# Performance work log

Hardware: AMD Instinct MI355X
Metric: run time of the kernel (lower is better)

## Reference

```python
import jax, jax.numpy as jnp
import numpy as np

H, W = 512, 512
K = 10
N_ACTIONS = 8
HID1, HID2, HIDP = 32, 64, 32
# 8-neighborhood directions (i_dot, j_dot), as in env.DIRS
DIRS = [(-1, -1), (-1, 0), (-1, 1), (0, -1), (0, 1), (1, -1), (1, 0), (1, 1)]


def setup_inputs() -> dict:
    key = jax.random.key(0)
    ks = jax.random.split(key, 16)
    n_state = H * W
    w = lambda k, shape: (jax.random.normal(k, shape, dtype=jnp.float32) * 0.02)
    return {
        "x": jax.random.uniform(ks[0], (3, H, W), dtype=jnp.float32),
        "pos": jax.random.randint(ks[1], (2,), 0, H, dtype=jnp.int32),
        "W1": w(ks[2], (HID1, 3 * n_state)), "b1": jnp.zeros((HID1,), jnp.float32),
        "W2": w(ks[3], (HID2, HID1)), "b2": jnp.zeros((HID2,), jnp.float32),
        "Wro": w(ks[4], (n_state, HID2)), "bro": jnp.zeros((n_state,), jnp.float32),
        "Wri": w(ks[5], (n_state, HID2)), "bri": jnp.zeros((n_state,), jnp.float32),
        "Wp": w(ks[6], (n_state, HID2)), "bp": jnp.zeros((n_state,), jnp.float32),
        "Wpol": w(ks[7], (HIDP, 4 * n_state)), "bpol": jnp.zeros((HIDP,), jnp.float32),
        "Whead": w(ks[8], (N_ACTIONS, HIDP)), "bhead": jnp.zeros((N_ACTIONS,), jnp.float32),
    }


def reference(x, pos, W1, b1, W2, b2, Wro, bro, Wri, bri, Wp, bp, Wpol, bpol, Whead, bhead):
    state = x.reshape(-1)  # (3*H*W,)
    h = jax.nn.relu(W1 @ state + b1)
    h = jax.nn.relu(W2 @ h + b2)
    r_out = jax.nn.sigmoid(Wro @ h + bro).reshape(H, W)
    r_in = jax.nn.sigmoid(Wri @ h + bri).reshape(H, W)
    p = jax.nn.sigmoid(Wp @ h + bp).reshape(H, W)

    p_pad = jnp.pad(p, 1)
    rin_pad = jnp.pad(r_in, 1)
    rout_pad = jnp.pad(r_out, 1)

    def step(v, _):
        v_pad = jnp.pad(v, 1)  # (H+2, W+2)
        cands = []
        for i_dot, j_dot in DIRS:
            xs = j_dot + 1  # note: original code uses j_dot along axis 0
            ys = i_dot + 1
            cands.append(
                v_pad[xs:xs + H, ys:ys + W] * p_pad[xs:xs + H, ys:ys + W]
                + rin_pad[xs:xs + H, ys:ys + W] - rout_pad[xs:xs + H, ys:ys + W]
            )
        return jnp.max(jnp.stack(cands, 0), axis=0), None

    v, _ = jax.lax.scan(step, jnp.zeros((H, W), jnp.float32), None, length=K)

    inp_pol = jnp.concatenate([v.reshape(-1), state])  # (4*H*W,)
    logits = Whead @ jax.nn.relu(Wpol @ inp_pol + bpol) + bhead
    action_prob = jax.nn.softmax(logits, axis=-1)
    state_value = v[pos[0], pos[1]]
    return action_prob, state_value
```

## Files before the change

### kernel.cpp

```cpp
#include <hip/hip_runtime.h>

#define HW 512
#define NSTATE (HW * HW)
#define NC4_X 196608
#define NC4_POLROW 262144
#define NC4_V 65536

#define SEG4 1024
#define NSEG_MV 192
#define NSEG_PV 64
#define SPAN_ROP 1024

#define WS_PART1 0
#define WS_PARTPX 6144
#define WS_PARTPV 12288
#define WS_H2 14336
#define WS_P 14400
#define WS_RD (WS_P + NSTATE)
#define WS_V (WS_RD + NSTATE)

#define SGB __builtin_amdgcn_sched_group_barrier

__global__ __launch_bounds__(256) void mv_dual(
    const float4* __restrict__ W1, const float4* __restrict__ Wpol,
    const float4* __restrict__ x, float* __restrict__ part1,
    float* __restrict__ partPx) {
  __shared__ float4 xs[SEG4];
  int b = blockIdx.x;
  int m = b >= 1536;
  if (m) b -= 1536;
  int q = b / NSEG_MV, s = b - q * NSEG_MV;
  int tid = threadIdx.x, wave = tid >> 6, lane = tid & 63;
  const float4* __restrict__ xseg = x + (size_t)s * SEG4;
#pragma unroll
  for (int k = 0; k < 4; ++k) xs[tid + k * 256] = xseg[tid + k * 256];
  __syncthreads();
  int row = q * 4 + wave;
  const float4* __restrict__ wrow =
      (m ? Wpol + NC4_V + (size_t)row * NC4_POLROW
         : W1 + (size_t)row * NC4_X) +
      (size_t)s * SEG4 + lane;
  float acc = 0.f;
#pragma unroll
  for (int bt = 0; bt < 2; ++bt) {
    float4 w[8];
#pragma unroll
    for (int j = 0; j < 8; ++j) w[j] = wrow[bt * 512 + j * 64];
    SGB(0x020, 8, 0);
    float4 xv[8];
#pragma unroll
    for (int j = 0; j < 8; ++j) xv[j] = xs[bt * 512 + j * 64 + lane];
#pragma unroll
    for (int j = 0; j < 8; ++j)
      acc += w[j].x * xv[j].x + w[j].y * xv[j].y + w[j].z * xv[j].z +
             w[j].w * xv[j].w;
  }
  acc += __shfl_xor(acc, 32);
  acc += __shfl_xor(acc, 16);
  acc += __shfl_xor(acc, 8);
  acc += __shfl_xor(acc, 4);
  acc += __shfl_xor(acc, 2);
  acc += __shfl_xor(acc, 1);
  if (lane == 0) (m ? partPx : part1)[s * 32 + row] = acc;
}

__global__ __launch_bounds__(256) void mv_polv(
    const float4* __restrict__ Wpol, const float4* __restrict__ v,
    float* __restrict__ partPv) {
  __shared__ float4 xs[SEG4];
  int b = blockIdx.x;
  int q = b / NSEG_PV, s = b - q * NSEG_PV;
  int tid = threadIdx.x, wave = tid >> 6, lane = tid & 63;
  const float4* __restrict__ vseg = v + (size_t)s * SEG4;
#pragma unroll
  for (int k = 0; k < 4; ++k) xs[tid + k * 256] = vseg[tid + k * 256];
  __syncthreads();
  int row = q * 4 + wave;
  const float4* __restrict__ wrow =
      Wpol + (size_t)row * NC4_POLROW + (size_t)s * SEG4 + lane;
  float acc = 0.f;
#pragma unroll
  for (int bt = 0; bt < 2; ++bt) {
    float4 w[8];
#pragma unroll
    for (int j = 0; j < 8; ++j) w[j] = wrow[bt * 512 + j * 64];
    SGB(0x020, 8, 0);
    float4 xv[8];
#pragma unroll
    for (int j = 0; j < 8; ++j) xv[j] = xs[bt * 512 + j * 64 + lane];
#pragma unroll
    for (int j = 0; j < 8; ++j)
      acc += w[j].x * xv[j].x + w[j].y * xv[j].y + w[j].z * xv[j].z +
             w[j].w * xv[j].w;
  }
  acc += __shfl_xor(acc, 32);
  acc += __shfl_xor(acc, 16);
  acc += __shfl_xor(acc, 8);
  acc += __shfl_xor(acc, 4);
  acc += __shfl_xor(acc, 2);
  acc += __shfl_xor(acc, 1);
  if (lane == 0) partPv[s * 32 + row] = acc;
}

__global__ __launch_bounds__(1024) void finish_h(
    const float* __restrict__ partials, const float* __restrict__ b1,
    const float* __restrict__ W2, const float* __restrict__ b2,
    float* __restrict__ h2out) {
  __shared__ float red[32][32];
  __shared__ float h1[32];
  int tid = threadIdx.x;
  int row = tid & 31, grp = tid >> 5;
  float s = 0.f;
  for (int b = grp; b < NSEG_MV; b += 32) s += partials[b * 32 + row];
  red[grp][row] = s;
  __syncthreads();
  if (tid < 32) {
    float t = b1[tid];
    for (int g = 0; g < 32; ++g) t += red[g][tid];
    h1[tid] = fmaxf(t, 0.f);
  }
  __syncthreads();
  if (tid < 64) {
    float t = b2[tid];
    for (int k = 0; k < 32; ++k) t += W2[tid * 32 + k] * h1[k];
    h2out[tid] = fmaxf(t, 0.f);
  }
}

__global__ __launch_bounds__(256) void rop_kernel(
    const float4* __restrict__ Wro4, const float* __restrict__ bro,
    const float4* __restrict__ Wri4, const float* __restrict__ bri,
    const float4* __restrict__ Wp4, const float* __restrict__ bp,
    const float* __restrict__ h2, float* __restrict__ p_out,
    float* __restrict__ rd_out) {
  __shared__ float dots[4][3][64];
  int tid = threadIdx.x;
  int wave = tid >> 6, lane = tid & 63;
  int grp = lane >> 4;
  float4 h4 = ((const float4*)h2)[lane & 15];
  int span = blockIdx.x * 4 + wave;
  size_t base = (size_t)span * SPAN_ROP;
  const float4* mats[3] = {Wro4, Wri4, Wp4};
#pragma unroll
  for (int m = 0; m < 3; ++m) {
    const float4* __restrict__ W = mats[m] + base + lane;
#pragma unroll
    for (int batch = 0; batch < 2; ++batch) {
      float4 w[8];
#pragma unroll
      for (int j = 0; j < 8; ++j) w[j] = W[(batch * 8 + j) * 64];
      SGB(0x020, 8, 0);
      float part[8];
#pragma unroll
      for (int j = 0; j < 8; ++j)
        part[j] = w[j].x * h4.x + w[j].y * h4.y + w[j].z * h4.z + w[j].w * h4.w;
#pragma unroll
      for (int j = 0; j < 8; ++j) {
        part[j] += __shfl_xor(part[j], 8);
        part[j] += __shfl_xor(part[j], 4);
        part[j] += __shfl_xor(part[j], 2);
        part[j] += __shfl_xor(part[j], 1);
      }
      if ((lane & 15) == 0) {
#pragma unroll
        for (int j = 0; j < 8; ++j)
          dots[wave][m][(batch * 8 + j) * 4 + grp] = part[j];
      }
    }
  }
  __syncthreads();
  int o = blockIdx.x * 256 + tid;
  float dro = dots[tid >> 6][0][tid & 63] + bro[o];
  float dri = dots[tid >> 6][1][tid & 63] + bri[o];
  float dp = dots[tid >> 6][2][tid & 63] + bp[o];
  float sro = 1.f / (1.f + __expf(-dro));
  float sri = 1.f / (1.f + __expf(-dri));
  float pv = 1.f / (1.f + __expf(-dp));
  p_out[o] = pv;
  rd_out[o] = sri - sro;
}

#define TILE 16
#define HALO 10
#define LR 36
__global__ __launch_bounds__(256) void valiter_kernel(
    const float* __restrict__ p, const float* __restrict__ rd,
    float* __restrict__ vout) {
  __shared__ float u[LR + 2][LR + 3];
  __shared__ float pp[LR][LR + 1];
  __shared__ float rr[LR][LR + 1];
  __shared__ float vv[LR][LR + 1];
  int tid = threadIdx.x;
  int ti = blockIdx.x >> 5, tj = blockIdx.x & 31;
  int gi0 = ti * TILE - HALO, gj0 = tj * TILE - HALO;
  for (int idx = tid; idx < (LR + 2) * (LR + 3); idx += 256)
    ((float*)u)[idx] = 0.f;
  for (int idx = tid; idx < LR * LR; idx += 256) {
    int i = idx / LR, j = idx % LR;
    int gi = gi0 + i, gj = gj0 + j;
    bool ok = (gi >= 0) & (gi < HW) & (gj >= 0) & (gj < HW);
    pp[i][j] = ok ? p[gi * HW + gj] : 0.f;
    rr[i][j] = ok ? rd[gi * HW + gj] : 0.f;
    vv[i][j] = 0.f;
  }
  __syncthreads();
  for (int k = 0; k < 10; ++k) {
#pragma unroll
    for (int idx = tid; idx < LR * LR; idx += 256) {
      int i = idx / LR, j = idx % LR;
      u[i + 1][j + 1] = vv[i][j] * pp[i][j] + rr[i][j];
    }
    __syncthreads();
#pragma unroll
    for (int idx = tid; idx < LR * LR; idx += 256) {
      int i = idx / LR, j = idx % LR;
      float m = u[i][j];
      m = fmaxf(m, u[i][j + 1]);
      m = fmaxf(m, u[i][j + 2]);
      m = fmaxf(m, u[i + 1][j]);
      m = fmaxf(m, u[i + 1][j + 2]);
      m = fmaxf(m, u[i + 2][j]);
      m = fmaxf(m, u[i + 2][j + 1]);
      m = fmaxf(m, u[i + 2][j + 2]);
      vv[i][j] = m;
    }
    __syncthreads();
  }
  if (tid < TILE * TILE) {
    int a = tid >> 4, b = tid & 15;
    vout[(ti * TILE + a) * HW + tj * TILE + b] = vv[HALO + a][HALO + b];
  }
}

__global__ __launch_bounds__(1024) void finish_pol(
    const float* __restrict__ partPx, const float* __restrict__ partPv,
    const float* __restrict__ bpol, const float* __restrict__ Whead,
    const float* __restrict__ bhead, const float* __restrict__ v,
    const int* __restrict__ pos, float* __restrict__ out) {
  __shared__ float red[32][32];
  __shared__ float hp[32];
  __shared__ float logits[8];
  int tid = threadIdx.x;
  int row = tid & 31, grp = tid >> 5;
  float s = 0.f;
  for (int b = grp; b < NSEG_MV; b += 32) s += partPx[b * 32 + row];
  for (int b = grp; b < NSEG_PV; b += 32) s += partPv[b * 32 + row];
  red[grp][row] = s;
  __syncthreads();
  if (tid < 32) {
    float t = bpol[tid];
    for (int g = 0; g < 32; ++g) t += red[g][tid];
    hp[tid] = fmaxf(t, 0.f);
  }
  __syncthreads();
  if (tid < 8) {
    float t = bhead[tid];
    for (int k = 0; k < 32; ++k) t += Whead[tid * 32 + k] * hp[k];
    logits[tid] = t;
  }
  __syncthreads();
  if (tid == 0) {
    float mx = logits[0];
    for (int j = 1; j < 8; ++j) mx = fmaxf(mx, logits[j]);
    float e[8], sum = 0.f;
    for (int j = 0; j < 8; ++j) {
      e[j] = __expf(logits[j] - mx);
      sum += e[j];
    }
    for (int j = 0; j < 8; ++j) out[j] = e[j] / sum;
    out[8] = v[pos[0] * HW + pos[1]];
  }
}

extern "C" void kernel_launch(void* const* d_in, const int* in_sizes, int n_in,
                              void* d_out, int out_size, void* d_ws,
                              size_t ws_size, hipStream_t stream) {
  const float* x = (const float*)d_in[0];
  const int* pos = (const int*)d_in[1];
  const float* W1 = (const float*)d_in[2];
  const float* b1 = (const float*)d_in[3];
  const float* W2 = (const float*)d_in[4];
  const float* b2 = (const float*)d_in[5];
  const float* Wro = (const float*)d_in[6];
  const float* bro = (const float*)d_in[7];
  const float* Wri = (const float*)d_in[8];
  const float* bri = (const float*)d_in[9];
  const float* Wp = (const float*)d_in[10];
  const float* bp = (const float*)d_in[11];
  const float* Wpol = (const float*)d_in[12];
  const float* bpol = (const float*)d_in[13];
  const float* Whead = (const float*)d_in[14];
  const float* bhead = (const float*)d_in[15];
  float* ws = (float*)d_ws;
  float* out = (float*)d_out;

  float* part1 = ws + WS_PART1;
  float* partPx = ws + WS_PARTPX;
  float* partPv = ws + WS_PARTPV;
  float* h2 = ws + WS_H2;
  float* pbuf = ws + WS_P;
  float* rdbuf = ws + WS_RD;
  float* vbuf = ws + WS_V;

  mv_dual<<<3072, 256, 0, stream>>>((const float4*)W1, (const float4*)Wpol,
                                    (const float4*)x, part1, partPx);
  finish_h<<<1, 1024, 0, stream>>>(part1, b1, W2, b2, h2);
  rop_kernel<<<1024, 256, 0, stream>>>((const float4*)Wro, bro,
                                       (const float4*)Wri, bri,
                                       (const float4*)Wp, bp, h2, pbuf, rdbuf);
  valiter_kernel<<<1024, 256, 0, stream>>>(pbuf, rdbuf, vbuf);
  mv_polv<<<512, 256, 0, stream>>>((const float4*)Wpol, (const float4*)vbuf,
                                   partPv);
  finish_pol<<<1, 1024, 0, stream>>>(partPx, partPv, bpol, Whead, bhead, vbuf,
                                     pos, out);
}
```

Measured before the change: 121.1 us.

## Move Wpol-x matvec into rop kernel and drop shared-memory staging of x

The Wpol·x partial matvec moves out of the first kernel and into the Wro/Wri/Wp projection kernel as extra blocks. The W1 matvec launch then shrinks and sits less on the critical path before finish_h, and the Wpol work fills the otherwise light rop launch. Each wave now reads its own x chunk straight from global memory instead of a block-shared LDS copy, which removes the __syncthreads. The cost is redundant x reads, which should mostly hit in cache. Partial indexing is remapped so that one wave handles one chunk per row.

```diff
diff --git a/kernel.cpp b/kernel.cpp
--- a/kernel.cpp
+++ b/kernel.cpp
@@ -6,9 +6,9 @@
 #define NC4_POLROW 262144
 #define NC4_V 65536
 
-#define SEG4 1024
-#define NSEG_MV 192
-#define NSEG_PV 64
+#define CH4 1024
+#define NCH_X 192
+#define NCH_V 64
 #define SPAN_ROP 1024
 
 #define WS_PART1 0
@@ -21,85 +21,48 @@
 
 #define SGB __builtin_amdgcn_sched_group_barrier
 
-__global__ __launch_bounds__(256) void mv_dual(
-    const float4* __restrict__ W1, const float4* __restrict__ Wpol,
-    const float4* __restrict__ x, float* __restrict__ part1,
-    float* __restrict__ partPx) {
-  __shared__ float4 xs[SEG4];
-  int b = blockIdx.x;
-  int m = b >= 1536;
-  if (m) b -= 1536;
-  int q = b / NSEG_MV, s = b - q * NSEG_MV;
-  int tid = threadIdx.x, wave = tid >> 6, lane = tid & 63;
-  const float4* __restrict__ xseg = x + (size_t)s * SEG4;
-#pragma unroll
-  for (int k = 0; k < 4; ++k) xs[tid + k * 256] = xseg[tid + k * 256];
-  __syncthreads();
-  int row = q * 4 + wave;
-  const float4* __restrict__ wrow =
-      (m ? Wpol + NC4_V + (size_t)row * NC4_POLROW
-         : W1 + (size_t)row * NC4_X) +
-      (size_t)s * SEG4 + lane;
+__device__ __forceinline__ float wred(float a) {
+  a += __shfl_xor(a, 32);
+  a += __shfl_xor(a, 16);
+  a += __shfl_xor(a, 8);
+  a += __shfl_xor(a, 4);
+  a += __shfl_xor(a, 2);
+  a += __shfl_xor(a, 1);
+  return a;
+}
+
+__device__ __forceinline__ float span_dot(const float4* __restrict__ wp,
+                                          const float4* __restrict__ xp) {
   float acc = 0.f;
 #pragma unroll
   for (int bt = 0; bt < 2; ++bt) {
-    float4 w[8];
-#pragma unroll
-    for (int j = 0; j < 8; ++j) w[j] = wrow[bt * 512 + j * 64];
-    SGB(0x020, 8, 0);
-    float4 xv[8];
-#pragma unroll
-    for (int j = 0; j < 8; ++j) xv[j] = xs[bt * 512 + j * 64 + lane];
+    float4 w[8], xv[8];
+#pragma unroll
+    for (int j = 0; j < 8; ++j) w[j] = wp[bt * 512 + j * 64];
+#pragma unroll
+    for (int j = 0; j < 8; ++j) xv[j] = xp[bt * 512 + j * 64];
+    SGB(0x020, 16, 0);
 #pragma unroll
     for (int j = 0; j < 8; ++j)
       acc += w[j].x * xv[j].x + w[j].y * xv[j].y + w[j].z * xv[j].z +
              w[j].w * xv[j].w;
   }
-  acc += __shfl_xor(acc, 32);
-  acc += __shfl_xor(acc, 16);
-  acc += __shfl_xor(acc, 8);
-  acc += __shfl_xor(acc, 4);
-  acc += __shfl_xor(acc, 2);
-  acc += __shfl_xor(acc, 1);
-  if (lane == 0) (m ? partPx : part1)[s * 32 + row] = acc;
-}
-
-__global__ __launch_bounds__(256) void mv_polv(
-    const float4* __restrict__ Wpol, const float4* __restrict__ v,
-    float* __restrict__ partPv) {
-  __shared__ float4 xs[SEG4];
+  return acc;
+}
+
+__global__ __launch_bounds__(256) void mv_w1(const float4* __restrict__ W1,
+                                             const float4* __restrict__ x,
+                                             float* __restrict__ part1) {
   int b = blockIdx.x;
-  int q = b / NSEG_PV, s = b - q * NSEG_PV;
+  int row = b / 48, cb = b - row * 48;
   int tid = threadIdx.x, wave = tid >> 6, lane = tid & 63;
-  const float4* __restrict__ vseg = v + (size_t)s * SEG4;
-#pragma unroll
-  for (int k = 0; k < 4; ++k) xs[tid + k * 256] = vseg[tid + k * 256];
-  __syncthreads();
-  int row = q * 4 + wave;
-  const float4* __restrict__ wrow =
-      Wpol + (size_t)row * NC4_POLROW + (size_t)s * SEG4 + lane;
-  float acc = 0.f;
-#pragma unroll
-  for (int bt = 0; bt < 2; ++bt) {
-    float4 w[8];
-#pragma unroll
-    for (int j = 0; j < 8; ++j) w[j] = wrow[bt * 512 + j * 64];
-    SGB(0x020, 8, 0);
-    float4 xv[8];
-#pragma unroll
-    for (int j = 0; j < 8; ++j) xv[j] = xs[bt * 512 + j * 64 + lane];
-#pragma unroll
-    for (int j = 0; j < 8; ++j)
-      acc += w[j].x * xv[j].x + w[j].y * xv[j].y + w[j].z * xv[j].z +
-             w[j].w * xv[j].w;
-  }
-  acc += __shfl_xor(acc, 32);
-  acc += __shfl_xor(acc, 16);
-  acc += __shfl_xor(acc, 8);
-  acc += __shfl_xor(acc, 4);
-  acc += __shfl_xor(acc, 2);
-  acc += __shfl_xor(acc, 1);
-  if (lane == 0) partPv[s * 32 + row] = acc;
+  int ch = cb * 4 + wave;
+  const float4* __restrict__ wp =
+      W1 + (size_t)row * NC4_X + (size_t)ch * CH4 + lane;
+  const float4* __restrict__ xp = x + (size_t)ch * CH4 + lane;
+  float acc = span_dot(wp, xp);
+  acc = wred(acc);
+  if (lane == 0) part1[ch * 32 + row] = acc;
 }
 
 __global__ __launch_bounds__(1024) void finish_h(
@@ -111,7 +74,7 @@
   int tid = threadIdx.x;
   int row = tid & 31, grp = tid >> 5;
   float s = 0.f;
-  for (int b = grp; b < NSEG_MV; b += 32) s += partials[b * 32 + row];
+  for (int b = grp; b < NCH_X; b += 32) s += partials[b * 32 + row];
   red[grp][row] = s;
   __syncthreads();
   if (tid < 32) {
@@ -127,15 +90,28 @@
   }
 }
 
-__global__ __launch_bounds__(256) void rop_kernel(
+__global__ __launch_bounds__(256) void ropx_kernel(
     const float4* __restrict__ Wro4, const float* __restrict__ bro,
     const float4* __restrict__ Wri4, const float* __restrict__ bri,
     const float4* __restrict__ Wp4, const float* __restrict__ bp,
     const float* __restrict__ h2, float* __restrict__ p_out,
-    float* __restrict__ rd_out) {
+    float* __restrict__ rd_out, const float4* __restrict__ Wpol,
+    const float4* __restrict__ x, float* __restrict__ partPx) {
   __shared__ float dots[4][3][64];
   int tid = threadIdx.x;
   int wave = tid >> 6, lane = tid & 63;
+  if (blockIdx.x >= 1024) {
+    int bb = blockIdx.x - 1024;
+    int row = bb / 48, cb = bb - row * 48;
+    int ch = cb * 4 + wave;
+    const float4* __restrict__ wp =
+        Wpol + (size_t)row * NC4_POLROW + NC4_V + (size_t)ch * CH4 + lane;
+    const float4* __restrict__ xp = x + (size_t)ch * CH4 + lane;
+    float acc = span_dot(wp, xp);
+    acc = wred(acc);
+    if (lane == 0) partPx[ch * 32 + row] = acc;
+    return;
+  }
   int grp = lane >> 4;
   float4 h4 = ((const float4*)h2)[lane & 15];
   int span = blockIdx.x * 4 + wave;
@@ -232,6 +208,21 @@
   }
 }
 
+__global__ __launch_bounds__(256) void mv_polv(const float4* __restrict__ Wpol,
+                                               const float4* __restrict__ v,
+                                               float* __restrict__ partPv) {
+  int b = blockIdx.x;
+  int row = b / 16, cb = b - row * 16;
+  int tid = threadIdx.x, wave = tid >> 6, lane = tid & 63;
+  int ch = cb * 4 + wave;
+  const float4* __restrict__ wp =
+      Wpol + (size_t)row * NC4_POLROW + (size_t)ch * CH4 + lane;
+  const float4* __restrict__ xp = v + (size_t)ch * CH4 + lane;
+  float acc = span_dot(wp, xp);
+  acc = wred(acc);
+  if (lane == 0) partPv[ch * 32 + row] = acc;
+}
+
 __global__ __launch_bounds__(1024) void finish_pol(
     const float* __restrict__ partPx, const float* __restrict__ partPv,
     const float* __restrict__ bpol, const float* __restrict__ Whead,
@@ -243,8 +234,8 @@
   int tid = threadIdx.x;
   int row = tid & 31, grp = tid >> 5;
   float s = 0.f;
-  for (int b = grp; b < NSEG_MV; b += 32) s += partPx[b * 32 + row];
-  for (int b = grp; b < NSEG_PV; b += 32) s += partPv[b * 32 + row];
+  for (int b = grp; b < NCH_X; b += 32) s += partPx[b * 32 + row];
+  for (int b = grp; b < NCH_V; b += 32) s += partPv[b * 32 + row];
   red[grp][row] = s;
   __syncthreads();
   if (tid < 32) {
@@ -302,12 +293,11 @@
   float* rdbuf = ws + WS_RD;
   float* vbuf = ws + WS_V;
 
-  mv_dual<<<3072, 256, 0, stream>>>((const float4*)W1, (const float4*)Wpol,
-                                    (const float4*)x, part1, partPx);
+  mv_w1<<<1536, 256, 0, stream>>>((const float4*)W1, (const float4*)x, part1);
   finish_h<<<1, 1024, 0, stream>>>(part1, b1, W2, b2, h2);
-  rop_kernel<<<1024, 256, 0, stream>>>((const float4*)Wro, bro,
-                                       (const float4*)Wri, bri,
-                                       (const float4*)Wp, bp, h2, pbuf, rdbuf);
+  ropx_kernel<<<2560, 256, 0, stream>>>(
+      (const float4*)Wro, bro, (const float4*)Wri, bri, (const float4*)Wp, bp,
+      h2, pbuf, rdbuf, (const float4*)Wpol, (const float4*)x, partPx);
   valiter_kernel<<<1024, 256, 0, stream>>>(pbuf, rdbuf, vbuf);
   mv_polv<<<512, 256, 0, stream>>>((const float4*)Wpol, (const float4*)vbuf,
                                    partPv);
```

New measurement: 125.5 us. +3.7%, slower.
